# Kernel optimization log

Measured on AMD Instinct MI355X. Metric: run time of the kernel, lower is better.

## Reference

```python
import jax, jax.numpy as jnp
import numpy as np

H = 16  # num heads


def setup_inputs() -> dict:
    key = jax.random.key(0)
    k1, k2, k3 = jax.random.split(key, 3)
    L, N, E = 2048, 4, 1024
    x = jax.random.normal(k1, (L, N, E), dtype=jnp.float32)
    wqkv = jax.random.normal(k2, (3 * E, E), dtype=jnp.float32) * 0.02
    wout = jax.random.normal(k3, (E, E), dtype=jnp.float32) * 0.02
    return {"x": x, "wqkv": wqkv, "wout": wout}


def reference(x, wqkv, wout):
    L, N, E = x.shape
    d = E // H
    scale = d ** (-0.5)
    # qkv projection: [L, N, 3E]
    qkv = jnp.einsum('lne,fe->lnf', x, wqkv)
    q, k, v = jnp.split(qkv, 3, axis=-1)
    # reshape to [N*H, L, d]
    def to_bld(t):
        return t.reshape(L, N * H, d).transpose(1, 0, 2)
    q = to_bld(q) * scale
    k = to_bld(k)
    v = to_bld(v)
    # full LxL scores (faithful to the naive implementation)
    attn = jnp.einsum('bld,bmd->blm', q, k)  # [N*H, L, L]
    causal = jnp.tril(jnp.ones((L, L), dtype=bool))
    attn = jnp.where(causal[None, :, :], attn, jnp.float32(-10000.0))
    attn = jax.nn.softmax(attn, axis=-1)
    # dropout = 0.0 / eval mode -> no-op
    out = jnp.einsum('blm,bmd->bld', attn, v)  # [N*H, L, d]
    out = out.transpose(1, 0, 2).reshape(L, N, E)
    out = jnp.einsum('lne,fe->lnf', out, wout)
    return jnp.sum(out)
```

## Files before the change

### kernel.cpp

```cpp
#include <hip/hip_runtime.h>
#include <hip/hip_bf16.h>

#define LSEQ 2048
#define NB   4
#define EMB  1024
#define NH   16
#define DH   64
#define BH   (NB*NH)
#define SCALE 0.125f
#define CCH  8

typedef unsigned short ushort8 __attribute__((ext_vector_type(8)));
typedef __attribute__((ext_vector_type(8))) short bf16x8;
typedef __attribute__((ext_vector_type(4))) float f32x4;
typedef __attribute__((ext_vector_type(16))) float f32x16;

__device__ __forceinline__ unsigned short f_to_bf(float f) {
    unsigned int u = __float_as_uint(f);
    return (unsigned short)((u + 0x7fffu + ((u >> 16) & 1u)) >> 16);
}

__device__ __forceinline__ void gload_lds16(const void* g, void* l) {
    __builtin_amdgcn_global_load_lds(
        (const __attribute__((address_space(1))) unsigned int*)g,
        (__attribute__((address_space(3))) unsigned int*)l, 16, 0, 0);
}

__global__ __launch_bounds__(256) void tobf16_kernel(const float* __restrict__ in,
                                                     unsigned short* __restrict__ out, int n8) {
    int i = blockIdx.x * 256 + threadIdx.x;
    if (i >= n8) return;
    const float4* p = reinterpret_cast<const float4*>(in) + (size_t)i * 2;
    float4 a = p[0], b = p[1];
    ushort8 o;
    o[0] = f_to_bf(a.x); o[1] = f_to_bf(a.y); o[2] = f_to_bf(a.z); o[3] = f_to_bf(a.w);
    o[4] = f_to_bf(b.x); o[5] = f_to_bf(b.y); o[6] = f_to_bf(b.z); o[7] = f_to_bf(b.w);
    reinterpret_cast<ushort8*>(out)[i] = o;
}

__global__ __launch_bounds__(256) void wsum_part_kernel(const float* __restrict__ wout,
                                                        float* __restrict__ wpart) {
    int fc = blockIdx.x >> 2;
    int e  = (blockIdx.x & 3) * 256 + threadIdx.x;
    float s = 0.f;
    #pragma unroll 8
    for (int f = fc * 32; f < fc * 32 + 32; ++f) s += wout[(size_t)f * EMB + e];
    wpart[(size_t)fc * EMB + e] = s;
}
__global__ __launch_bounds__(256) void wsum_final_kernel(const float* __restrict__ wpart,
                                                         float* __restrict__ wsum) {
    int e = blockIdx.x * 256 + threadIdx.x;
    float s = 0.f;
    #pragma unroll
    for (int c = 0; c < 32; ++c) s += wpart[(size_t)c * EMB + e];
    wsum[e] = s;
}

__global__ void wveff_kernel(const float* __restrict__ wqkv, const float* __restrict__ wsum,
                             float* __restrict__ wveff) {
    int idx = blockIdx.x * 256 + threadIdx.x;
    int h = idx >> 10, e = idx & 1023;
    float s = 0.f;
    #pragma unroll 8
    for (int j = 0; j < DH; ++j)
        s += wqkv[(size_t)(2 * EMB + h * DH + j) * EMB + e] * wsum[h * DH + j];
    wveff[idx] = s;
}

__global__ __launch_bounds__(256) void vw_kernel(const float* __restrict__ x,
                                                 const float* __restrict__ wveff,
                                                 float* __restrict__ vw) {
    int wave = threadIdx.x >> 6;
    int lane = threadIdx.x & 63;
    int r = blockIdx.x * 4 + wave;
    int n = r & 3, l = r >> 2;
    float acc[NH] = {};
    for (int e = lane; e < EMB; e += 64) {
        float xe = x[(size_t)r * EMB + e];
        #pragma unroll
        for (int h = 0; h < NH; ++h) acc[h] += xe * wveff[h * EMB + e];
    }
    #pragma unroll
    for (int h = 0; h < NH; ++h) {
        float v = acc[h];
        #pragma unroll
        for (int off = 32; off > 0; off >>= 1) v += __shfl_down(v, off, 64);
        if (lane == 0) vw[(size_t)(n * NH + h) * LSEQ + l] = v;
    }
}

#define PBM 128
#define PBN 128
#define PBK 64
__global__ __launch_bounds__(256) void proj_mfma(const unsigned short* __restrict__ xb,
                                                 const unsigned short* __restrict__ wb,
                                                 unsigned short* __restrict__ qws,
                                                 unsigned short* __restrict__ kws) {
    __shared__ unsigned short SMEM[PBM * PBK + PBN * PBK];
    unsigned short* As = SMEM;
    unsigned short* Bs = SMEM + PBM * PBK;
    const int tid  = threadIdx.x;
    const int lane = tid & 63;
    const int wid  = tid >> 6;
    const int wr   = wid >> 1, wc = wid & 1;
    const int d  = blockIdx.x;
    const int w  = (d & 7) * 128 + (d >> 3);
    const int r0 = (w >> 4) * PBM;
    const int c0 = (w & 15) * PBN;
    const int col  = lane & 15, g = lane >> 4;

    f32x4 acc[4][4];
    #pragma unroll
    for (int m = 0; m < 4; ++m)
        #pragma unroll
        for (int n = 0; n < 4; ++n) acc[m][n] = f32x4{0.f, 0.f, 0.f, 0.f};

    const int srow = lane >> 3;
    const int sj   = ((lane & 7) ^ (lane >> 3)) * 8;

    for (int k0 = 0; k0 < EMB; k0 += PBK) {
        #pragma unroll
        for (int i = 0; i < 4; ++i) {
            int seg = wid * 4 + i;
            gload_lds16(&xb[(size_t)(r0 + seg * 8 + srow) * EMB + k0 + sj],
                        &As[seg * 8 * PBK]);
            gload_lds16(&wb[(size_t)(c0 + seg * 8 + srow) * EMB + k0 + sj],
                        &Bs[seg * 8 * PBK]);
        }
        __syncthreads();
        #pragma unroll
        for (int kk = 0; kk < 2; ++kk) {
            bf16x8 af[4], bff[4];
            #pragma unroll
            for (int m = 0; m < 4; ++m) {
                int row = wr * 64 + m * 16 + col;
                af[m] = *reinterpret_cast<const bf16x8*>(
                    &As[row * PBK + (((kk * 4 + g) ^ (row & 7)) * 8)]);
            }
            #pragma unroll
            for (int n = 0; n < 4; ++n) {
                int row = wc * 64 + n * 16 + col;
                bff[n] = *reinterpret_cast<const bf16x8*>(
                    &Bs[row * PBK + (((kk * 4 + g) ^ (row & 7)) * 8)]);
            }
            #pragma unroll
            for (int m = 0; m < 4; ++m)
                #pragma unroll
                for (int n = 0; n < 4; ++n)
                    acc[m][n] = __builtin_amdgcn_mfma_f32_16x16x32_bf16(af[m], bff[n], acc[m][n], 0, 0, 0);
        }
        __syncthreads();
    }

    const float scl = (c0 < EMB) ? SCALE : 1.0f;
    #pragma unroll
    for (int m = 0; m < 4; ++m) {
        #pragma unroll
        for (int n = 0; n < 4; ++n) {
            #pragma unroll
            for (int j = 0; j < 4; ++j) {
                int row = wr * 64 + m * 16 + g * 4 + j;
                int cc  = wc * 64 + n * 16 + col;
                SMEM[row * 128 + (((cc >> 3) ^ (row & 7)) * 8) + (cc & 7)] =
                    f_to_bf(acc[m][n][j] * scl);
            }
        }
    }
    __syncthreads();
    #pragma unroll
    for (int pass = 0; pass < 8; ++pass) {
        int unit = pass * 32 + (tid >> 3);
        int r    = unit >> 1;
        int hsel = unit & 1;
        int pg   = (tid & 7) ^ (r & 7);
        ushort8 u = *reinterpret_cast<const ushort8*>(
            &SMEM[r * 128 + (hsel * 8 + (tid & 7)) * 8]);
        int rg = r0 + r;
        int nb = rg & 3, l = rg >> 2;
        int cbase = c0 + hsel * 64;
        unsigned short* dstp;
        if (c0 < EMB) {
            dstp = &qws[((size_t)(nb * NH + (cbase >> 6)) * LSEQ + l) * DH];
        } else {
            int c2 = cbase - EMB;
            dstp = &kws[((size_t)(nb * NH + (c2 >> 6)) * LSEQ + l) * DH];
        }
        *reinterpret_cast<ushort8*>(dstp + pg * 8) = u;
    }
}

__device__ __forceinline__ void lds_kfrag(const unsigned short* Ks, int ti, int m, int half,
                                          bf16x8* kf) {
    const char* base = reinterpret_cast<const char*>(Ks);
    #pragma unroll
    for (int kk = 0; kk < 4; ++kk) {
        int byte = ti * 4096 + m * 128 + ((half * 16 + kk * 32) ^ ((m & 7) << 4));
        kf[kk] = *reinterpret_cast<const bf16x8*>(base + byte);
    }
}
__device__ __forceinline__ f32x16 mfma_tile(const bf16x8* kf, const bf16x8* qf) {
    f32x16 acc;
    #pragma unroll
    for (int j = 0; j < 16; ++j) acc[j] = 0.f;
    #pragma unroll
    for (int kk = 0; kk < 4; ++kk)
        acc = __builtin_amdgcn_mfma_f32_32x32x16_bf16(kf[kk], qf[kk], acc, 0, 0, 0);
    return acc;
}
__device__ __forceinline__ void expacc(const f32x16& acc, const float* vt, int half,
                                       float& z, float& o) {
    #pragma unroll
    for (int q = 0; q < 4; ++q) {
        float4 v4 = *reinterpret_cast<const float4*>(&vt[8 * q + 4 * half]);
        float vvq[4] = {v4.x, v4.y, v4.z, v4.w};
        #pragma unroll
        for (int j = 0; j < 4; ++j) {
            float p = __expf(acc[4 * q + j] - 16.0f);
            z += p;
            o += p * vvq[j];
        }
    }
}
__device__ __forceinline__ void expacc_diag(const f32x16& acc, const float* vt, int half,
                                            int row, float& z, float& o) {
    #pragma unroll
    for (int q = 0; q < 4; ++q) {
        float4 v4 = *reinterpret_cast<const float4*>(&vt[8 * q + 4 * half]);
        float vvq[4] = {v4.x, v4.y, v4.z, v4.w};
        #pragma unroll
        for (int j = 0; j < 4; ++j) {
            int mrow = j + 8 * q + 4 * half;
            float p = __expf(acc[4 * q + j] - 16.0f);
            p = (mrow <= row) ? p : 0.f;
            z += p;
            o += p * vvq[j];
        }
    }
}

__global__ __launch_bounds__(512) void attn_mfma(const unsigned short* __restrict__ qws,
                                                 const unsigned short* __restrict__ kws,
                                                 const float* __restrict__ vw,
                                                 float2* __restrict__ zopart) {
    __shared__ unsigned short Ks[CCH * 2048];
    __shared__ float vt[CCH][32];
    const int tid = threadIdx.x;
    const int b   = blockIdx.x & 63;
    const int c   = blockIdx.x >> 6;

    {
        int ti = tid >> 6, lane = tid & 63;
        int row = lane >> 1, hb = lane & 1;
        const unsigned short* src = &kws[((size_t)b * LSEQ + (c + CCH * ti) * 32 + row) * DH + hb * 32];
        char* dst = reinterpret_cast<char*>(Ks) + ti * 4096 + row * 128;
        #pragma unroll
        for (int s = 0; s < 4; ++s) {
            ushort8 u = *reinterpret_cast<const ushort8*>(src + s * 8);
            *reinterpret_cast<ushort8*>(dst + ((hb * 64 + s * 16) ^ ((row & 7) << 4))) = u;
        }
        if (tid < 256) vt[tid >> 5][tid & 31] =
            vw[(size_t)b * LSEQ + (c + CCH * (tid >> 5)) * 32 + (tid & 31)];
    }
    __syncthreads();

    const int wid  = tid >> 6;
    const int lane = tid & 63;
    const int row  = lane & 31;
    const int half = lane >> 5;

    #pragma unroll
    for (int k = 0; k < 8; ++k) {
        const int lb = 8 * k + wid;
        const int nfull = (lb > c) ? ((lb - c + 7) >> 3) : 0;
        const bool has_diag = ((lb & 7) == c);
        float z = 0.f, o = 0.f;
        if (nfull > 0 || has_diag) {
            const unsigned short* qbase = &qws[((size_t)b * LSEQ + lb * 32 + row) * DH + 8 * half];
            bf16x8 qf[4];
            #pragma unroll
            for (int kk = 0; kk < 4; ++kk)
                qf[kk] = *reinterpret_cast<const bf16x8*>(qbase + kk * 16);

            int ti = 0;
            for (; ti + 1 < nfull; ti += 2) {
                bf16x8 ka[4], kc[4];
                lds_kfrag(Ks, ti, row, half, ka);
                lds_kfrag(Ks, ti + 1, row, half, kc);
                __builtin_amdgcn_s_setprio(1);
                f32x16 accA = mfma_tile(ka, qf);
                f32x16 accB = mfma_tile(kc, qf);
                __builtin_amdgcn_s_setprio(0);
                expacc(accA, &vt[ti][0], half, z, o);
                expacc(accB, &vt[ti + 1][0], half, z, o);
            }
            if (ti < nfull) {
                bf16x8 ka[4];
                lds_kfrag(Ks, ti, row, half, ka);
                f32x16 accA = mfma_tile(ka, qf);
                expacc(accA, &vt[ti][0], half, z, o);
            }
            if (has_diag) {
                const int td = nfull;
                bf16x8 ka[4];
                lds_kfrag(Ks, td, row, half, ka);
                f32x16 accA = mfma_tile(ka, qf);
                expacc_diag(accA, &vt[td][0], half, row, z, o);
            }
            z += __shfl_xor(z, 32, 64);
            o += __shfl_xor(o, 32, 64);
        }
        if (half == 0)
            zopart[((size_t)(b * 64 + lb) * CCH + c) * 32 + row] = float2{z, o};
    }
}

__global__ __launch_bounds__(256) void attn_combine(const float2* __restrict__ zopart,
                                                    float* __restrict__ partials) {
    __shared__ float red[256];
    const int t = threadIdx.x;
    const int e = blockIdx.x * 256 + t;
    const int bl = e >> 5, col = e & 31;
    float z = 0.f, o = 0.f;
    #pragma unroll
    for (int c = 0; c < CCH; ++c) {
        float2 p = zopart[((size_t)bl * CCH + c) * 32 + col];
        z += p.x; o += p.y;
    }
    red[t] = o / z;
    __syncthreads();
    for (int sh = 128; sh > 0; sh >>= 1) {
        if (t < sh) red[t] += red[t + sh];
        __syncthreads();
    }
    if (t == 0) partials[blockIdx.x] = red[0];
}

__global__ void reduce_kernel(const float* __restrict__ partials, float* __restrict__ out) {
    __shared__ float red[256];
    int t = threadIdx.x;
    red[t] = partials[t] + partials[t + 256];
    __syncthreads();
    for (int sh = 128; sh > 0; sh >>= 1) {
        if (t < sh) red[t] += red[t + sh];
        __syncthreads();
    }
    if (t == 0) out[0] = red[0];
}

extern "C" void kernel_launch(void* const* d_in, const int* in_sizes, int n_in,
                              void* d_out, int out_size, void* d_ws, size_t ws_size,
                              hipStream_t stream) {
    const float* x    = (const float*)d_in[0];
    const float* wqkv = (const float*)d_in[1];
    const float* wout = (const float*)d_in[2];
    float* out = (float*)d_out;

    unsigned short* qws = (unsigned short*)d_ws;
    unsigned short* kws = qws + (size_t)BH * LSEQ * DH;
    unsigned short* xb  = kws + (size_t)BH * LSEQ * DH;
    unsigned short* wb  = xb + (size_t)LSEQ * NB * EMB;
    float* vw       = (float*)(wb + (size_t)2 * EMB * EMB);
    float* wsum     = vw + (size_t)BH * LSEQ;
    float* wveff    = wsum + EMB;
    float* partials = wveff + NH * EMB;
    float* wpart    = partials + 1024;
    float2* zopart  = (float2*)xb;

    hipLaunchKernelGGL(tobf16_kernel, dim3(LSEQ * NB * EMB / 8 / 256), dim3(256), 0, stream,
                       x, xb, LSEQ * NB * EMB / 8);
    hipLaunchKernelGGL(tobf16_kernel, dim3(2 * EMB * EMB / 8 / 256), dim3(256), 0, stream,
                       wqkv, wb, 2 * EMB * EMB / 8);
    hipLaunchKernelGGL(wsum_part_kernel,  dim3(128), dim3(256), 0, stream, wout, wpart);
    hipLaunchKernelGGL(wsum_final_kernel, dim3(EMB / 256), dim3(256), 0, stream, wpart, wsum);
    hipLaunchKernelGGL(wveff_kernel,  dim3(NH * EMB / 256), dim3(256), 0, stream, wqkv, wsum, wveff);
    hipLaunchKernelGGL(vw_kernel,     dim3(LSEQ * NB / 4), dim3(256), 0, stream, x, wveff, vw);
    hipLaunchKernelGGL(proj_mfma,     dim3(1024), dim3(256), 0, stream,
                       xb, wb, qws, kws);
    hipLaunchKernelGGL(attn_mfma,     dim3(BH * CCH), dim3(512), 0, stream,
                       qws, kws, vw, zopart);
    hipLaunchKernelGGL(attn_combine,  dim3(512), dim3(256), 0, stream, zopart, partials);
    hipLaunchKernelGGL(reduce_kernel, dim3(1), dim3(256), 0, stream, partials, out);
}
```

Before: 137.4 us.

## Fuse x bf16 conversion into vw kernel and double-buffer projection GEMM

The separate x-to-bf16 conversion kernel is removed; vw_kernel now loads each row of x once with float4 loads, writes the bf16 copy, and computes the per-head dot products from registers. The projection GEMM gains a second LDS buffer so the async global-to-LDS load of the next K tile overlaps MFMA work on the current tile. This saves one full pass over x and a launch, and targets load latency in the GEMM. In exchange, the GEMM's LDS use doubles, which may reduce occupancy.

```diff
diff --git a/kernel.cpp b/kernel.cpp
--- a/kernel.cpp
+++ b/kernel.cpp
@@ -69,16 +69,39 @@
 
 __global__ __launch_bounds__(256) void vw_kernel(const float* __restrict__ x,
                                                  const float* __restrict__ wveff,
-                                                 float* __restrict__ vw) {
+                                                 float* __restrict__ vw,
+                                                 unsigned short* __restrict__ xb) {
     int wave = threadIdx.x >> 6;
     int lane = threadIdx.x & 63;
     int r = blockIdx.x * 4 + wave;
     int n = r & 3, l = r >> 2;
-    float acc[NH] = {};
-    for (int e = lane; e < EMB; e += 64) {
-        float xe = x[(size_t)r * EMB + e];
-        #pragma unroll
-        for (int h = 0; h < NH; ++h) acc[h] += xe * wveff[h * EMB + e];
+    int e0 = lane * 16;
+    float xv[16];
+    const float4* xp = reinterpret_cast<const float4*>(&x[(size_t)r * EMB + e0]);
+    #pragma unroll
+    for (int i = 0; i < 4; ++i) {
+        float4 v = xp[i];
+        xv[4*i+0] = v.x; xv[4*i+1] = v.y; xv[4*i+2] = v.z; xv[4*i+3] = v.w;
+    }
+    ushort8 u0, u1;
+    #pragma unroll
+    for (int j = 0; j < 8; ++j) u0[j] = f_to_bf(xv[j]);
+    #pragma unroll
+    for (int j = 0; j < 8; ++j) u1[j] = f_to_bf(xv[8 + j]);
+    ushort8* xbp = reinterpret_cast<ushort8*>(&xb[(size_t)r * EMB + e0]);
+    xbp[0] = u0; xbp[1] = u1;
+
+    float acc[NH];
+    #pragma unroll
+    for (int h = 0; h < NH; ++h) {
+        const float4* wp = reinterpret_cast<const float4*>(&wveff[h * EMB + e0]);
+        float s = 0.f;
+        #pragma unroll
+        for (int i = 0; i < 4; ++i) {
+            float4 w = wp[i];
+            s += xv[4*i+0]*w.x + xv[4*i+1]*w.y + xv[4*i+2]*w.z + xv[4*i+3]*w.w;
+        }
+        acc[h] = s;
     }
     #pragma unroll
     for (int h = 0; h < NH; ++h) {
@@ -92,13 +115,54 @@
 #define PBM 128
 #define PBN 128
 #define PBK 64
+#define BUFS ((PBM + PBN) * PBK)
+
+__device__ __forceinline__ void proj_stage(const unsigned short* __restrict__ xb,
+                                           const unsigned short* __restrict__ wb,
+                                           unsigned short* As, unsigned short* Bs,
+                                           int r0, int c0, int k0, int wid, int srow, int sj) {
+    #pragma unroll
+    for (int i = 0; i < 4; ++i) {
+        int seg = wid * 4 + i;
+        gload_lds16(&xb[(size_t)(r0 + seg * 8 + srow) * EMB + k0 + sj], &As[seg * 8 * PBK]);
+        gload_lds16(&wb[(size_t)(c0 + seg * 8 + srow) * EMB + k0 + sj], &Bs[seg * 8 * PBK]);
+    }
+}
+
+__device__ __forceinline__ void proj_compute(const unsigned short* As, const unsigned short* Bs,
+                                             int wr, int wc, int col, int g, f32x4 (&acc)[4][4]) {
+    #pragma unroll
+    for (int kk = 0; kk < 2; ++kk) {
+        bf16x8 af[4], bff[4];
+        #pragma unroll
+        for (int m = 0; m < 4; ++m) {
+            int row = wr * 64 + m * 16 + col;
+            af[m] = *reinterpret_cast<const bf16x8*>(
+                &As[row * PBK + (((kk * 4 + g) ^ (row & 7)) * 8)]);
+        }
+        #pragma unroll
+        for (int n = 0; n < 4; ++n) {
+            int row = wc * 64 + n * 16 + col;
+            bff[n] = *reinterpret_cast<const bf16x8*>(
+                &Bs[row * PBK + (((kk * 4 + g) ^ (row & 7)) * 8)]);
+        }
+        #pragma unroll
+        for (int m = 0; m < 4; ++m)
+            #pragma unroll
+            for (int n = 0; n < 4; ++n)
+                acc[m][n] = __builtin_amdgcn_mfma_f32_16x16x32_bf16(af[m], bff[n], acc[m][n], 0, 0, 0);
+    }
+}
+
 __global__ __launch_bounds__(256) void proj_mfma(const unsigned short* __restrict__ xb,
                                                  const unsigned short* __restrict__ wb,
                                                  unsigned short* __restrict__ qws,
                                                  unsigned short* __restrict__ kws) {
-    __shared__ unsigned short SMEM[PBM * PBK + PBN * PBK];
-    unsigned short* As = SMEM;
-    unsigned short* Bs = SMEM + PBM * PBK;
+    __shared__ unsigned short SMEM[2 * BUFS];
+    unsigned short* As0 = SMEM;
+    unsigned short* Bs0 = SMEM + PBM * PBK;
+    unsigned short* As1 = SMEM + BUFS;
+    unsigned short* Bs1 = As1 + PBM * PBK;
     const int tid  = threadIdx.x;
     const int lane = tid & 63;
     const int wid  = tid >> 6;
@@ -118,37 +182,16 @@
     const int srow = lane >> 3;
     const int sj   = ((lane & 7) ^ (lane >> 3)) * 8;
 
-    for (int k0 = 0; k0 < EMB; k0 += PBK) {
-        #pragma unroll
-        for (int i = 0; i < 4; ++i) {
-            int seg = wid * 4 + i;
-            gload_lds16(&xb[(size_t)(r0 + seg * 8 + srow) * EMB + k0 + sj],
-                        &As[seg * 8 * PBK]);
-            gload_lds16(&wb[(size_t)(c0 + seg * 8 + srow) * EMB + k0 + sj],
-                        &Bs[seg * 8 * PBK]);
-        }
+    proj_stage(xb, wb, As0, Bs0, r0, c0, 0, wid, srow, sj);
+    __syncthreads();
+    #pragma unroll 1
+    for (int t = 0; t < 16; t += 2) {
+        proj_stage(xb, wb, As1, Bs1, r0, c0, (t + 1) * PBK, wid, srow, sj);
+        proj_compute(As0, Bs0, wr, wc, col, g, acc);
         __syncthreads();
-        #pragma unroll
-        for (int kk = 0; kk < 2; ++kk) {
-            bf16x8 af[4], bff[4];
-            #pragma unroll
-            for (int m = 0; m < 4; ++m) {
-                int row = wr * 64 + m * 16 + col;
-                af[m] = *reinterpret_cast<const bf16x8*>(
-                    &As[row * PBK + (((kk * 4 + g) ^ (row & 7)) * 8)]);
-            }
-            #pragma unroll
-            for (int n = 0; n < 4; ++n) {
-                int row = wc * 64 + n * 16 + col;
-                bff[n] = *reinterpret_cast<const bf16x8*>(
-                    &Bs[row * PBK + (((kk * 4 + g) ^ (row & 7)) * 8)]);
-            }
-            #pragma unroll
-            for (int m = 0; m < 4; ++m)
-                #pragma unroll
-                for (int n = 0; n < 4; ++n)
-                    acc[m][n] = __builtin_amdgcn_mfma_f32_16x16x32_bf16(af[m], bff[n], acc[m][n], 0, 0, 0);
-        }
+        if (t + 2 < 16)
+            proj_stage(xb, wb, As0, Bs0, r0, c0, (t + 2) * PBK, wid, srow, sj);
+        proj_compute(As1, Bs1, wr, wc, col, g, acc);
         __syncthreads();
     }
 
@@ -366,14 +409,12 @@
     float* wpart    = partials + 1024;
     float2* zopart  = (float2*)xb;
 
-    hipLaunchKernelGGL(tobf16_kernel, dim3(LSEQ * NB * EMB / 8 / 256), dim3(256), 0, stream,
-                       x, xb, LSEQ * NB * EMB / 8);
     hipLaunchKernelGGL(tobf16_kernel, dim3(2 * EMB * EMB / 8 / 256), dim3(256), 0, stream,
                        wqkv, wb, 2 * EMB * EMB / 8);
     hipLaunchKernelGGL(wsum_part_kernel,  dim3(128), dim3(256), 0, stream, wout, wpart);
     hipLaunchKernelGGL(wsum_final_kernel, dim3(EMB / 256), dim3(256), 0, stream, wpart, wsum);
     hipLaunchKernelGGL(wveff_kernel,  dim3(NH * EMB / 256), dim3(256), 0, stream, wqkv, wsum, wveff);
-    hipLaunchKernelGGL(vw_kernel,     dim3(LSEQ * NB / 4), dim3(256), 0, stream, x, wveff, vw);
+    hipLaunchKernelGGL(vw_kernel,     dim3(LSEQ * NB / 4), dim3(256), 0, stream, x, wveff, vw, xb);
     hipLaunchKernelGGL(proj_mfma,     dim3(1024), dim3(256), 0, stream,
                        xb, wb, qws, kws);
     hipLaunchKernelGGL(attn_mfma,     dim3(BH * CCH), dim3(512), 0, stream,
```

Measured after the change: 167.9 us. +22.2%, slower.
